# Kernel optimization log

Measured on AMD Instinct MI355X. Metric: run time of the kernel, lower is better.

The kernel has to match this reference:

```python
import jax, jax.numpy as jnp
import numpy as np

B, S, D, H, DH, F = 4, 2048, 1024, 16, 64, 4096
EPS = 1e-5


def setup_inputs() -> dict:
    key = jax.random.key(0)
    ks = jax.random.split(key, 8)
    std = 0.02
    return {
        "src": jax.random.normal(ks[0], (B, S, D), dtype=jnp.float32),
        # per-head Q/K/V projections, stacked: [H, D, DH]
        "Wq": jax.random.normal(ks[1], (H, D, DH), dtype=jnp.float32) * std,
        "bq": jnp.zeros((H, DH), dtype=jnp.float32),
        "Wk": jax.random.normal(ks[2], (H, D, DH), dtype=jnp.float32) * std,
        "bk": jnp.zeros((H, DH), dtype=jnp.float32),
        "Wv": jax.random.normal(ks[3], (H, D, DH), dtype=jnp.float32) * std,
        "bv": jnp.zeros((H, DH), dtype=jnp.float32),
        "Wo": jax.random.normal(ks[4], (H * DH, D), dtype=jnp.float32) * std,
        "bo": jnp.zeros((D,), dtype=jnp.float32),
        "ln1_w": jnp.ones((D,), dtype=jnp.float32),
        "ln1_b": jnp.zeros((D,), dtype=jnp.float32),
        "W1": jax.random.normal(ks[5], (D, F), dtype=jnp.float32) * std,
        "b1": jnp.zeros((F,), dtype=jnp.float32),
        "W2": jax.random.normal(ks[6], (F, D), dtype=jnp.float32) * std,
        "b2": jnp.zeros((D,), dtype=jnp.float32),
        "ln2_w": jnp.ones((D,), dtype=jnp.float32),
        "ln2_b": jnp.zeros((D,), dtype=jnp.float32),
    }


def _layernorm(x, w, b):
    m = jnp.mean(x, axis=-1, keepdims=True)
    v = jnp.mean(jnp.square(x - m), axis=-1, keepdims=True)
    return (x - m) * jax.lax.rsqrt(v + EPS) * w + b


def reference(src, Wq, bq, Wk, bk, Wv, bv, Wo, bo, ln1_w, ln1_b, W1, b1, W2, b2, ln2_w, ln2_b):
    # Per-head projections, batched over heads: [B,H,S,DH]
    q = jnp.einsum('bsd,hde->bhse', src, Wq) + bq[None, :, None, :]
    k = jnp.einsum('bsd,hde->bhse', src, Wk) + bk[None, :, None, :]
    v = jnp.einsum('bsd,hde->bhse', src, Wv) + bv[None, :, None, :]
    scale = jnp.asarray(DH, src.dtype) ** 0.5
    scores = jnp.einsum('bhqe,bhke->bhqk', q, k) / scale  # [B,H,S,S]
    attn = jax.nn.softmax(scores, axis=-1)
    ctx = jnp.einsum('bhqk,bhke->bhqe', attn, v)  # [B,H,S,DH]
    # concat heads along feature dim (matches torch.cat over head outputs)
    ctx = ctx.transpose(0, 2, 1, 3).reshape(src.shape[0], src.shape[1], H * DH)
    attn_out = ctx @ Wo + bo
    x = _layernorm(src + attn_out, ln1_w, ln1_b)
    ffn = jax.nn.relu(x @ W1 + b1) @ W2 + b2
    return _layernorm(x + ffn, ln2_w, ln2_b)
```

## Files before the change

### kernel.cpp

```cpp
#include <hip/hip_runtime.h>
#include <stdint.h>


typedef unsigned short u16;
typedef __attribute__((ext_vector_type(8))) short short8;
typedef __attribute__((ext_vector_type(4))) float f32x4;
typedef __attribute__((ext_vector_type(16))) float f32x16;

__device__ __forceinline__ u16 f2bf(float f) {
  union { float f; unsigned u; } v; v.f = f;
  unsigned r = (v.u + 0x7fffu + ((v.u >> 16) & 1u)) >> 16;
  return (u16)r;
}

__device__ __forceinline__ void gl_lds16(const u16* g, u16* l) {
  __builtin_amdgcn_global_load_lds(
      (const __attribute__((address_space(1))) unsigned int*)g,
      (__attribute__((address_space(3))) unsigned int*)l, 16, 0, 0);
}

__device__ __forceinline__ unsigned cvtpk(float lo, float hi) {
  unsigned r;
  asm("v_cvt_pk_bf16_f32 %0, %1, %2" : "=v"(r) : "v"(lo), "v"(hi));
  return r;
}
__device__ __forceinline__ void pl32_swap(unsigned& a, unsigned& b) {
  asm("v_permlane32_swap_b32 %0, %1" : "+v"(a), "+v"(b));
}


__global__ __launch_bounds__(256) void transpose_cast(const float* __restrict__ W,
                                                      u16* __restrict__ WT,
                                                      int K, int N) {
  __shared__ u16 T[64 * 72];
  const int tid = threadIdx.x;
  const long n0 = (long)blockIdx.x * 64, k0 = (long)blockIdx.y * 64;
#pragma unroll
  for (int i = 0; i < 4; i++) {
    int c = tid + i * 256;
    int kr = c >> 4, nc = (c & 15) * 4;
    float4 v = *(const float4*)(W + (k0 + kr) * N + n0 + nc);
    T[(nc + 0) * 72 + kr] = f2bf(v.x);
    T[(nc + 1) * 72 + kr] = f2bf(v.y);
    T[(nc + 2) * 72 + kr] = f2bf(v.z);
    T[(nc + 3) * 72 + kr] = f2bf(v.w);
  }
  __syncthreads();
#pragma unroll
  for (int i = 0; i < 2; i++) {
    int c = tid + i * 256;
    int nr = c >> 3, kc = (c & 7) * 8;
    *(uint4*)(WT + (n0 + nr) * K + k0 + kc) = *(const uint4*)(T + nr * 72 + kc);
  }
}

__global__ __launch_bounds__(256) void transpose_cast_qkv(const float* __restrict__ Wq,
                                                          const float* __restrict__ Wk,
                                                          const float* __restrict__ Wv,
                                                          u16* __restrict__ WT) {
  __shared__ u16 T[64 * 72];
  const int tid = threadIdx.x;
  const int n0 = blockIdx.x * 64, k0 = blockIdx.y * 64;
  const float* W = (n0 < 1024) ? Wq : (n0 < 2048 ? Wk : Wv);
  const int h = (n0 & 1023) >> 6;
#pragma unroll
  for (int i = 0; i < 4; i++) {
    int c = tid + i * 256;
    int kr = c >> 4, ec = (c & 15) * 4;
    float4 v = *(const float4*)(W + ((long)h * 1024 + k0 + kr) * 64 + ec);
    T[(ec + 0) * 72 + kr] = f2bf(v.x);
    T[(ec + 1) * 72 + kr] = f2bf(v.y);
    T[(ec + 2) * 72 + kr] = f2bf(v.z);
    T[(ec + 3) * 72 + kr] = f2bf(v.w);
  }
  __syncthreads();
#pragma unroll
  for (int i = 0; i < 2; i++) {
    int c = tid + i * 256;
    int nr = c >> 3, kc = (c & 7) * 8;
    *(uint4*)(WT + ((long)(n0 + nr)) * 1024 + k0 + kc) = *(const uint4*)(T + nr * 72 + kc);
  }
}

__global__ __launch_bounds__(256) void cast_bf16(const float* __restrict__ x, u16* __restrict__ y) {
  const long i = ((long)blockIdx.x * 256 + threadIdx.x) * 8;
  float4 a = *(const float4*)(x + i);
  float4 b = *(const float4*)(x + i + 4);
  uint4 o;
  o.x = (unsigned)f2bf(a.x) | ((unsigned)f2bf(a.y) << 16);
  o.y = (unsigned)f2bf(a.z) | ((unsigned)f2bf(a.w) << 16);
  o.z = (unsigned)f2bf(b.x) | ((unsigned)f2bf(b.y) << 16);
  o.w = (unsigned)f2bf(b.z) | ((unsigned)f2bf(b.w) << 16);
  *(uint4*)(y + i) = o;
}

__global__ __launch_bounds__(256) void build_bcat(const float* __restrict__ bq,
                                                  const float* __restrict__ bk,
                                                  const float* __restrict__ bv,
                                                  float* __restrict__ bcat) {
  int i = blockIdx.x * 256 + threadIdx.x;
  const float* s = (i < 1024) ? bq : (i < 2048 ? bk : bv);
  bcat[i] = s[i & 1023];
}

#define GEMM_PROLOGUE                                                              \
  __shared__ __align__(16) u16 As[2][4096];                                        \
  __shared__ __align__(16) u16 Bs[2][4096];                                        \
  const int tid = threadIdx.x;                                                     \
  const int wave = tid >> 6, lane = tid & 63, quad = lane >> 4, l15 = lane & 15;   \
  const int wm = (wave >> 1) * 64, wn = (wave & 1) * 64;                           \
  const int id = blockIdx.x, xcd = id & 7, ii = id >> 3;                           \
  const long m0 = (long)(xcd * 8 + (ii & 7)) * 128, n0 = (long)(ii >> 3) * 128;    \
  const int srow = tid >> 2, sc = (tid & 3) ^ ((srow >> 1) & 3);                   \
  const u16* Ag = A + (m0 + srow) * K + sc * 8;                                    \
  const u16* Bg = B + (n0 + srow) * K + sc * 8;                                    \
  const int cx = (l15 >> 1) & 3;                                                   \
  f32x4 acc[4][4] = {};                                                            \
  gl_lds16(Ag, &As[0][tid * 8]);                                                   \
  gl_lds16(Ag + (long)64 * K, &As[0][tid * 8 + 2048]);                             \
  gl_lds16(Bg, &Bs[0][tid * 8]);                                                   \
  gl_lds16(Bg + (long)64 * K, &Bs[0][tid * 8 + 2048]);                             \
  for (int k0 = 0; k0 < K; k0 += 32) {                                             \
    __syncthreads();         \
    const int cur = (k0 >> 5) & 1;                                                 \
    if (k0 + 32 < K) {                                                             \
      gl_lds16(Ag + k0 + 32, &As[cur ^ 1][tid * 8]);                               \
      gl_lds16(Ag + (long)64 * K + k0 + 32, &As[cur ^ 1][tid * 8 + 2048]);         \
      gl_lds16(Bg + k0 + 32, &Bs[cur ^ 1][tid * 8]);                               \
      gl_lds16(Bg + (long)64 * K + k0 + 32, &Bs[cur ^ 1][tid * 8 + 2048]);         \
    }                                                                              \
    short8 af[4], bfr[4];                                                          \
    _Pragma("unroll") for (int t = 0; t < 4; t++)                                  \
        af[t] = *(const short8*)(&As[cur][(wm + t * 16 + l15) * 32 + (quad ^ cx) * 8]); \
    _Pragma("unroll") for (int t = 0; t < 4; t++)                                  \
        bfr[t] = *(const short8*)(&Bs[cur][(wn + t * 16 + l15) * 32 + (quad ^ cx) * 8]); \
    _Pragma("unroll") for (int i = 0; i < 4; i++)                                  \
        _Pragma("unroll") for (int j = 0; j < 4; j++)                              \
            acc[i][j] = __builtin_amdgcn_mfma_f32_16x16x32_bf16(af[i], bfr[j],     \
                                                                acc[i][j], 0, 0, 0); \
  }

template <int MODE>
__global__ __launch_bounds__(256) void gemm_bt(const u16* __restrict__ A, const u16* __restrict__ B,
                                               const float* __restrict__ bias, void* __restrict__ Cout,
                                               int K, int N) {
  GEMM_PROLOGUE
#pragma unroll
  for (int i = 0; i < 4; i++) {
#pragma unroll
    for (int j = 0; j < 4; j++) {
      const long col = n0 + wn + j * 16 + l15;
      const float bb = bias[col];
      const long rowb = m0 + wm + i * 16 + quad * 4;
#pragma unroll
      for (int r = 0; r < 4; r++) {
        float v = acc[i][j][r] + bb;
        if (MODE == 2) v = fmaxf(v, 0.f);
        if (MODE == 0)
          ((float*)Cout)[(rowb + r) * N + col] = v;
        else
          ((u16*)Cout)[(rowb + r) * N + col] = f2bf(v);
      }
    }
  }
}

template <int MODE>
__global__ __launch_bounds__(512) void gemm_bt_sk(const u16* __restrict__ A, const u16* __restrict__ B,
                                                  const float* __restrict__ bias, void* __restrict__ Cout,
                                                  int K, int N) {
  __shared__ __align__(16) u16 As[2][2][4096];
  __shared__ __align__(16) u16 Bs[2][2][4096];
  const int tid = threadIdx.x;
  const int wave = tid >> 6, lane = tid & 63, quad = lane >> 4, l15 = lane & 15;
  const int kh = wave >> 2, w4 = wave & 3;
  const int wm = (w4 >> 1) * 64, wn = (w4 & 1) * 64;
  const int id = blockIdx.x, xcd = id & 7, ii = id >> 3;
  const long m0 = (long)(xcd * 8 + (ii & 7)) * 128, n0 = (long)(ii >> 3) * 128;
  const int t = tid & 255;
  const int srow = t >> 2, sc = (t & 3) ^ ((srow >> 1) & 3);
  const int Kh = K >> 1;
  const u16* Ag = A + (m0 + srow) * K + kh * Kh + sc * 8;
  const u16* Bg = B + (n0 + srow) * K + kh * Kh + sc * 8;
  const int cx = (l15 >> 1) & 3;
  f32x4 acc[4][4] = {};
  gl_lds16(Ag, &As[kh][0][t * 8]);
  gl_lds16(Ag + (long)64 * K, &As[kh][0][t * 8 + 2048]);
  gl_lds16(Bg, &Bs[kh][0][t * 8]);
  gl_lds16(Bg + (long)64 * K, &Bs[kh][0][t * 8 + 2048]);
  for (int k0 = 0; k0 < Kh; k0 += 32) {
    __syncthreads();
    const int cur = (k0 >> 5) & 1;
    if (k0 + 32 < Kh) {
      gl_lds16(Ag + k0 + 32, &As[kh][cur ^ 1][t * 8]);
      gl_lds16(Ag + (long)64 * K + k0 + 32, &As[kh][cur ^ 1][t * 8 + 2048]);
      gl_lds16(Bg + k0 + 32, &Bs[kh][cur ^ 1][t * 8]);
      gl_lds16(Bg + (long)64 * K + k0 + 32, &Bs[kh][cur ^ 1][t * 8 + 2048]);
    }
    short8 af[4], bfr[4];
#pragma unroll
    for (int tt = 0; tt < 4; tt++)
      af[tt] = *(const short8*)(&As[kh][cur][(wm + tt * 16 + l15) * 32 + (quad ^ cx) * 8]);
#pragma unroll
    for (int tt = 0; tt < 4; tt++)
      bfr[tt] = *(const short8*)(&Bs[kh][cur][(wn + tt * 16 + l15) * 32 + (quad ^ cx) * 8]);
#pragma unroll
    for (int i = 0; i < 4; i++)
#pragma unroll
      for (int j = 0; j < 4; j++)
        acc[i][j] = __builtin_amdgcn_mfma_f32_16x16x32_bf16(af[i], bfr[j], acc[i][j], 0, 0, 0);
  }
  __syncthreads();
  float* red = (w4 & 2) ? (float*)Bs : (float*)As;
  float* myred = red + (w4 & 1) * 4096 + lane * 4;
  if (kh == 1) {
#pragma unroll
    for (int i = 0; i < 4; i++)
#pragma unroll
      for (int j = 0; j < 4; j++)
        *(f32x4*)(myred + (i * 4 + j) * 256) = acc[i][j];
  }
  __syncthreads();
  if (kh == 0) {
#pragma unroll
    for (int i = 0; i < 4; i++) {
#pragma unroll
      for (int j = 0; j < 4; j++) {
        const f32x4 o = *(const f32x4*)(myred + (i * 4 + j) * 256);
        const long col = n0 + wn + j * 16 + l15;
        const float bb = bias[col];
        const long rowb = m0 + wm + i * 16 + quad * 4;
#pragma unroll
        for (int r = 0; r < 4; r++) {
          float v = acc[i][j][r] + o[r] + bb;
          if (MODE == 2) v = fmaxf(v, 0.f);
          if (MODE == 0)
            ((float*)Cout)[(rowb + r) * N + col] = v;
          else
            ((u16*)Cout)[(rowb + r) * N + col] = f2bf(v);
        }
      }
    }
  }
}

__global__ __launch_bounds__(256) void gemm_qkv(const u16* __restrict__ A, const u16* __restrict__ B,
                                                const float* __restrict__ bias,
                                                u16* __restrict__ QKb, u16* __restrict__ Vt, int K) {
  GEMM_PROLOGUE
#pragma unroll
  for (int i = 0; i < 4; i++) {
#pragma unroll
    for (int j = 0; j < 4; j++) {
      const int col0 = (int)n0 + wn + j * 16;
      const int col = col0 + l15;
      const float bb = bias[col];
      const long rowb = m0 + wm + i * 16 + quad * 4;
      if (col0 < 1024) {
#pragma unroll
        for (int r = 0; r < 4; r++)
          QKb[(rowb + r) * 2048 + col] = f2bf((acc[i][j][r] + bb) * 0.1803368801f);
      } else if (col0 < 2048) {
#pragma unroll
        for (int r = 0; r < 4; r++)
          QKb[(rowb + r) * 2048 + col] = f2bf(acc[i][j][r] + bb);
      } else {
        const int ec = col - 2048;
        const int bq = (int)(rowb >> 11), s = (int)(rowb & 2047);
        uint2 p;
        p.x = (unsigned)f2bf(acc[i][j][0] + bb) | ((unsigned)f2bf(acc[i][j][1] + bb) << 16);
        p.y = (unsigned)f2bf(acc[i][j][2] + bb) | ((unsigned)f2bf(acc[i][j][3] + bb) << 16);
        *(uint2*)(Vt + ((long)(bq * 16 + (ec >> 6)) * 64 + (ec & 63)) * 2048 + s) = p;
      }
    }
  }
}


__device__ __forceinline__ void stage_tile(const u16* __restrict__ g, u16* __restrict__ lds, int tid) {
#pragma unroll
  for (int i = 0; i < 2; i++) {
    const int s = i * 256 + tid;
    const int r = s >> 3, cs = s & 7;
    const int c = cs ^ (r & 7);
    gl_lds16(g + (long)r * 2048 + c * 8, lds + s * 8);
  }
}
__device__ __forceinline__ short8 frag(const u16* __restrict__ buf, int row, int chunk) {
  const int slot = row * 8 + (chunk ^ (row & 7));
  return *(const short8*)(buf + slot * 8);
}

__global__ __launch_bounds__(256, 2) void flash_attn(const u16* __restrict__ QKb,
                                                     const u16* __restrict__ Vt,
                                                     u16* __restrict__ ctx) {
  __shared__ __align__(16) u16 Kbuf[2][4096];
  __shared__ __align__(16) u16 Vbuf[2][4096];
  const int tid = threadIdx.x, wave = tid >> 6, lane = tid & 63;
  const int l31 = lane & 31, hi = lane >> 5;
  const int bh = blockIdx.x, b = bh >> 4, h = bh & 15;
  const int qt = blockIdx.y;
  const long qbase = (long)b * 2048 + qt * 256 + wave * 64;
  const u16* Qg = QKb + qbase * 2048 + h * 64;
  const u16* Kg = QKb + ((long)b * 2048) * 2048 + 1024 + h * 64;
  const u16* Vg = Vt + (long)bh * 64 * 2048;

  short8 qf[2][4];
#pragma unroll
  for (int j = 0; j < 2; j++)
#pragma unroll
    for (int ks = 0; ks < 4; ks++)
      qf[j][ks] = *(const short8*)(Qg + (long)(j * 32 + l31) * 2048 + ks * 16 + hi * 8);

  f32x16 O[2][2] = {};
  float rs[2] = {0.f, 0.f};

  stage_tile(Kg, Kbuf[0], tid);
  stage_tile(Vg, Vbuf[0], tid);

  for (int kt = 0; kt < 32; kt++) {
    __syncthreads();
    if (kt < 31) {
      stage_tile(Kg + (long)(kt + 1) * 64 * 2048, Kbuf[(kt + 1) & 1], tid);
      stage_tile(Vg + (kt + 1) * 64, Vbuf[(kt + 1) & 1], tid);
    }
    const u16* Kb = Kbuf[kt & 1];
    const u16* Vb = Vbuf[kt & 1];

#pragma unroll
    for (int m = 0; m < 2; m++) {
      short8 ak[4];
#pragma unroll
      for (int ks = 0; ks < 4; ks++) ak[ks] = frag(Kb, m * 32 + l31, ks * 2 + hi);
      f32x16 S[2] = {};
#pragma unroll
      for (int ks = 0; ks < 4; ks++)
#pragma unroll
        for (int j = 0; j < 2; j++)
          S[j] = __builtin_amdgcn_mfma_f32_32x32x16_bf16(ak[ks], qf[j][ks], S[j], 0, 0, 0);

      short8 pf[2][2];
#pragma unroll
      for (int j = 0; j < 2; j++) {
#pragma unroll
        for (int r = 0; r < 16; r++) S[j][r] = __builtin_amdgcn_exp2f(S[j][r]);
        rs[j] += ((S[j][0] + S[j][1]) + (S[j][2] + S[j][3])) +
                 ((S[j][4] + S[j][5]) + (S[j][6] + S[j][7])) +
                 ((S[j][8] + S[j][9]) + (S[j][10] + S[j][11])) +
                 ((S[j][12] + S[j][13]) + (S[j][14] + S[j][15]));
        unsigned w0 = cvtpk(S[j][0], S[j][1]), w1 = cvtpk(S[j][2], S[j][3]);
        unsigned w2 = cvtpk(S[j][4], S[j][5]), w3 = cvtpk(S[j][6], S[j][7]);
        unsigned w4 = cvtpk(S[j][8], S[j][9]), w5 = cvtpk(S[j][10], S[j][11]);
        unsigned w6 = cvtpk(S[j][12], S[j][13]), w7 = cvtpk(S[j][14], S[j][15]);
        pl32_swap(w2, w0); pl32_swap(w3, w1);
        pl32_swap(w6, w4); pl32_swap(w7, w5);
        union { unsigned u[4]; short8 s8; } f0, f1;
        f0.u[0] = w0; f0.u[1] = w1; f0.u[2] = w2; f0.u[3] = w3;
        f1.u[0] = w4; f1.u[1] = w5; f1.u[2] = w6; f1.u[3] = w7;
        pf[j][0] = f0.s8; pf[j][1] = f1.s8;
      }

#pragma unroll
      for (int et = 0; et < 2; et++) {
        short8 av[2];
#pragma unroll
        for (int ks2 = 0; ks2 < 2; ks2++)
          av[ks2] = frag(Vb, et * 32 + l31, m * 4 + ks2 * 2 + hi);
#pragma unroll
        for (int j = 0; j < 2; j++)
#pragma unroll
          for (int ks2 = 0; ks2 < 2; ks2++)
            O[et][j] = __builtin_amdgcn_mfma_f32_32x32x16_bf16(av[ks2], pf[j][ks2],
                                                               O[et][j], 0, 0, 0);
      }
    }
  }

#pragma unroll
  for (int j = 0; j < 2; j++) rs[j] += __shfl_xor(rs[j], 32);
#pragma unroll
  for (int j = 0; j < 2; j++) {
    const float inv = 1.f / rs[j];
    const long row = qbase + j * 32 + l31;
#pragma unroll
    for (int et = 0; et < 2; et++)
#pragma unroll
      for (int g = 0; g < 4; g++) {
        const int e0 = et * 32 + g * 8 + hi * 4;
        uint2 p;
        p.x = (unsigned)f2bf(O[et][j][g * 4 + 0] * inv) |
              ((unsigned)f2bf(O[et][j][g * 4 + 1] * inv) << 16);
        p.y = (unsigned)f2bf(O[et][j][g * 4 + 2] * inv) |
              ((unsigned)f2bf(O[et][j][g * 4 + 3] * inv) << 16);
        *(uint2*)(ctx + row * 1024 + h * 64 + e0) = p;
      }
  }
}

template <bool WB>
__global__ __launch_bounds__(256) void add_ln(const float* __restrict__ a, const float* __restrict__ c,
                                              const float* __restrict__ w, const float* __restrict__ bias,
                                              float* __restrict__ xout, u16* __restrict__ xbf) {
  const int row = blockIdx.x, tid = threadIdx.x;
  const long off = (long)row * 1024 + tid * 4;
  float4 va = *(const float4*)(a + off);
  float4 vc = *(const float4*)(c + off);
  float4 s = {va.x + vc.x, va.y + vc.y, va.z + vc.z, va.w + vc.w};
  float sum = s.x + s.y + s.z + s.w;
  float sq = s.x * s.x + s.y * s.y + s.z * s.z + s.w * s.w;
#pragma unroll
  for (int o = 32; o > 0; o >>= 1) {
    sum += __shfl_xor(sum, o);
    sq += __shfl_xor(sq, o);
  }
  __shared__ float red[8];
  const int wave = tid >> 6;
  if ((tid & 63) == 0) { red[wave] = sum; red[wave + 4] = sq; }
  __syncthreads();
  sum = red[0] + red[1] + red[2] + red[3];
  sq = red[4] + red[5] + red[6] + red[7];
  const float mean = sum * (1.f / 1024.f);
  const float var = sq * (1.f / 1024.f) - mean * mean;
  const float rstd = rsqrtf(var + 1e-5f);
  float4 vw = *(const float4*)(w + tid * 4);
  float4 vb = *(const float4*)(bias + tid * 4);
  float4 y;
  y.x = (s.x - mean) * rstd * vw.x + vb.x;
  y.y = (s.y - mean) * rstd * vw.y + vb.y;
  y.z = (s.z - mean) * rstd * vw.z + vb.z;
  y.w = (s.w - mean) * rstd * vw.w + vb.w;
  *(float4*)(xout + off) = y;
  if (WB) {
    uint2 o2;
    o2.x = (unsigned)f2bf(y.x) | ((unsigned)f2bf(y.y) << 16);
    o2.y = (unsigned)f2bf(y.z) | ((unsigned)f2bf(y.w) << 16);
    *(uint2*)(xbf + off) = o2;
  }
}

extern "C" void kernel_launch(void* const* d_in, const int* in_sizes, int n_in,
                              void* d_out, int out_size, void* d_ws, size_t ws_size,
                              hipStream_t stream) {
  (void)in_sizes; (void)n_in; (void)out_size; (void)ws_size;
  const float* src = (const float*)d_in[0];
  const float* Wq = (const float*)d_in[1];
  const float* bq = (const float*)d_in[2];
  const float* Wk = (const float*)d_in[3];
  const float* bk = (const float*)d_in[4];
  const float* Wv = (const float*)d_in[5];
  const float* bv = (const float*)d_in[6];
  const float* Wo = (const float*)d_in[7];
  const float* bo = (const float*)d_in[8];
  const float* ln1w = (const float*)d_in[9];
  const float* ln1b = (const float*)d_in[10];
  const float* W1 = (const float*)d_in[11];
  const float* b1 = (const float*)d_in[12];
  const float* W2 = (const float*)d_in[13];
  const float* b2 = (const float*)d_in[14];
  const float* ln2w = (const float*)d_in[15];
  const float* ln2b = (const float*)d_in[16];

  char* ws = (char*)d_ws;
  u16* WqkvT = (u16*)(ws + 0);
  u16* WoT = (u16*)(ws + (6ul << 20));
  u16* W1T = (u16*)(ws + (8ul << 20));
  u16* W2T = (u16*)(ws + (16ul << 20));
  float* bcat = (float*)(ws + (24ul << 20));
  u16* srcb = (u16*)(ws + (25ul << 20));
  u16* QKb = (u16*)(ws + (41ul << 20));
  u16* Vt = (u16*)(ws + (73ul << 20));
  u16* ctxb = (u16*)(ws + (89ul << 20));
  float* x = (float*)(ws + (105ul << 20));
  u16* xb = (u16*)(ws + (137ul << 20));
  u16* hb = (u16*)(ws + (41ul << 20));
  float* out = (float*)d_out;

  transpose_cast_qkv<<<dim3(48, 16), 256, 0, stream>>>(Wq, Wk, Wv, WqkvT);
  transpose_cast<<<dim3(16, 16), 256, 0, stream>>>(Wo, WoT, 1024, 1024);
  transpose_cast<<<dim3(64, 16), 256, 0, stream>>>(W1, W1T, 1024, 4096);
  transpose_cast<<<dim3(16, 64), 256, 0, stream>>>(W2, W2T, 4096, 1024);
  cast_bf16<<<4096, 256, 0, stream>>>(src, srcb);
  build_bcat<<<12, 256, 0, stream>>>(bq, bk, bv, bcat);

  gemm_qkv<<<24 * 64, 256, 0, stream>>>(srcb, WqkvT, bcat, QKb, Vt, 1024);
  flash_attn<<<dim3(64, 8), 256, 0, stream>>>(QKb, Vt, ctxb);
  gemm_bt_sk<0><<<8 * 64, 512, 0, stream>>>(ctxb, WoT, bo, out, 1024, 1024);
  add_ln<true><<<8192, 256, 0, stream>>>(src, out, ln1w, ln1b, x, xb);
  gemm_bt<2><<<32 * 64, 256, 0, stream>>>(xb, W1T, b1, hb, 1024, 4096);
  gemm_bt_sk<0><<<8 * 64, 512, 0, stream>>>(hb, W2T, b2, out, 4096, 1024);
  add_ln<false><<<8192, 256, 0, stream>>>(x, out, ln2w, ln2b, out, nullptr);
}
```

Baseline: 511.6 us.

## Triple-buffer GEMM LDS staging with explicit vmcnt waits and hoist bias loads

Turns the 256-thread GEMM k-loop from double to triple buffering, so tiles are prefetched two iterations ahead. It waits on the outstanding global-to-LDS loads with an explicit s_waitcnt vmcnt plus a raw s_barrier, where it previously relied on __syncthreads. Bias values are now loaded before the k-loop instead of in the epilogue. The goal is to hide global load latency better, at the cost of more LDS per block (48KB), which may lower occupancy. It also depends on the vmcnt count matching exactly four loads per stage.

```diff
diff --git a/kernel.cpp b/kernel.cpp
--- a/kernel.cpp
+++ b/kernel.cpp
@@ -103,9 +103,9 @@
   bcat[i] = s[i & 1023];
 }
 
-#define GEMM_PROLOGUE                                                              \
-  __shared__ __align__(16) u16 As[2][4096];                                        \
-  __shared__ __align__(16) u16 Bs[2][4096];                                        \
+#define GEMM_SETUP                                                                 \
+  __shared__ __align__(16) u16 As[3][4096];                                        \
+  __shared__ __align__(16) u16 Bs[3][4096];                                        \
   const int tid = threadIdx.x;                                                     \
   const int wave = tid >> 6, lane = tid & 63, quad = lane >> 4, l15 = lane & 15;   \
   const int wm = (wave >> 1) * 64, wn = (wave & 1) * 64;                           \
@@ -114,47 +114,59 @@
   const int srow = tid >> 2, sc = (tid & 3) ^ ((srow >> 1) & 3);                   \
   const u16* Ag = A + (m0 + srow) * K + sc * 8;                                    \
   const u16* Bg = B + (n0 + srow) * K + sc * 8;                                    \
-  const int cx = (l15 >> 1) & 3;                                                   \
-  f32x4 acc[4][4] = {};                                                            \
-  gl_lds16(Ag, &As[0][tid * 8]);                                                   \
-  gl_lds16(Ag + (long)64 * K, &As[0][tid * 8 + 2048]);                             \
-  gl_lds16(Bg, &Bs[0][tid * 8]);                                                   \
-  gl_lds16(Bg + (long)64 * K, &Bs[0][tid * 8 + 2048]);                             \
+  const int cq = quad ^ ((l15 >> 1) & 3);                                          \
+  f32x4 acc[4][4] = {};
+
+#define GEMM_STAGE(b, kof)                                                         \
+  {                                                                                \
+    gl_lds16(Ag + (kof), &As[b][tid * 8]);                                         \
+    gl_lds16(Ag + (long)64 * K + (kof), &As[b][tid * 8 + 2048]);                   \
+    gl_lds16(Bg + (kof), &Bs[b][tid * 8]);                                         \
+    gl_lds16(Bg + (long)64 * K + (kof), &Bs[b][tid * 8 + 2048]);                   \
+  }
+
+#define GEMM_KLOOP                                                                 \
+  GEMM_STAGE(0, 0)                                                                 \
+  GEMM_STAGE(1, 32)                                                                \
+  int cur = 0;                                                                     \
   for (int k0 = 0; k0 < K; k0 += 32) {                                             \
-    __syncthreads();         \
-    const int cur = (k0 >> 5) & 1;                                                 \
-    if (k0 + 32 < K) {                                                             \
-      gl_lds16(Ag + k0 + 32, &As[cur ^ 1][tid * 8]);                               \
-      gl_lds16(Ag + (long)64 * K + k0 + 32, &As[cur ^ 1][tid * 8 + 2048]);         \
-      gl_lds16(Bg + k0 + 32, &Bs[cur ^ 1][tid * 8]);                               \
-      gl_lds16(Bg + (long)64 * K + k0 + 32, &Bs[cur ^ 1][tid * 8 + 2048]);         \
+    if (k0 + 32 < K) asm volatile("s_waitcnt vmcnt(4)" ::: "memory");              \
+    else asm volatile("s_waitcnt vmcnt(0)" ::: "memory");                          \
+    __builtin_amdgcn_s_barrier();                                                  \
+    if (k0 + 64 < K) {                                                             \
+      const int nb = cur == 0 ? 2 : cur - 1;                        \
+      GEMM_STAGE(nb, k0 + 64)                                                      \
     }                                                                              \
     short8 af[4], bfr[4];                                                          \
     _Pragma("unroll") for (int t = 0; t < 4; t++)                                  \
-        af[t] = *(const short8*)(&As[cur][(wm + t * 16 + l15) * 32 + (quad ^ cx) * 8]); \
+        af[t] = *(const short8*)(&As[cur][(wm + t * 16 + l15) * 32 + cq * 8]);     \
     _Pragma("unroll") for (int t = 0; t < 4; t++)                                  \
-        bfr[t] = *(const short8*)(&Bs[cur][(wn + t * 16 + l15) * 32 + (quad ^ cx) * 8]); \
+        bfr[t] = *(const short8*)(&Bs[cur][(wn + t * 16 + l15) * 32 + cq * 8]);    \
     _Pragma("unroll") for (int i = 0; i < 4; i++)                                  \
         _Pragma("unroll") for (int j = 0; j < 4; j++)                              \
             acc[i][j] = __builtin_amdgcn_mfma_f32_16x16x32_bf16(af[i], bfr[j],     \
                                                                 acc[i][j], 0, 0, 0); \
+    cur = cur == 2 ? 0 : cur + 1;                                                  \
   }
 
 template <int MODE>
 __global__ __launch_bounds__(256) void gemm_bt(const u16* __restrict__ A, const u16* __restrict__ B,
                                                const float* __restrict__ bias, void* __restrict__ Cout,
                                                int K, int N) {
-  GEMM_PROLOGUE
+  GEMM_SETUP
+  float bb[4];
+#pragma unroll
+  for (int j = 0; j < 4; j++) bb[j] = bias[n0 + wn + j * 16 + l15];
+  GEMM_KLOOP
 #pragma unroll
   for (int i = 0; i < 4; i++) {
 #pragma unroll
     for (int j = 0; j < 4; j++) {
       const long col = n0 + wn + j * 16 + l15;
-      const float bb = bias[col];
       const long rowb = m0 + wm + i * 16 + quad * 4;
 #pragma unroll
       for (int r = 0; r < 4; r++) {
-        float v = acc[i][j][r] + bb;
+        float v = acc[i][j][r] + bb[j];
         if (MODE == 2) v = fmaxf(v, 0.f);
         if (MODE == 0)
           ((float*)Cout)[(rowb + r) * N + col] = v;
@@ -247,29 +259,32 @@
 __global__ __launch_bounds__(256) void gemm_qkv(const u16* __restrict__ A, const u16* __restrict__ B,
                                                 const float* __restrict__ bias,
                                                 u16* __restrict__ QKb, u16* __restrict__ Vt, int K) {
-  GEMM_PROLOGUE
+  GEMM_SETUP
+  float bb[4];
+#pragma unroll
+  for (int j = 0; j < 4; j++) bb[j] = bias[n0 + wn + j * 16 + l15];
+  GEMM_KLOOP
 #pragma unroll
   for (int i = 0; i < 4; i++) {
 #pragma unroll
     for (int j = 0; j < 4; j++) {
       const int col0 = (int)n0 + wn + j * 16;
       const int col = col0 + l15;
-      const float bb = bias[col];
       const long rowb = m0 + wm + i * 16 + quad * 4;
       if (col0 < 1024) {
 #pragma unroll
         for (int r = 0; r < 4; r++)
-          QKb[(rowb + r) * 2048 + col] = f2bf((acc[i][j][r] + bb) * 0.1803368801f);
+          QKb[(rowb + r) * 2048 + col] = f2bf((acc[i][j][r] + bb[j]) * 0.1803368801f);
       } else if (col0 < 2048) {
 #pragma unroll
         for (int r = 0; r < 4; r++)
-          QKb[(rowb + r) * 2048 + col] = f2bf(acc[i][j][r] + bb);
+          QKb[(rowb + r) * 2048 + col] = f2bf(acc[i][j][r] + bb[j]);
       } else {
         const int ec = col - 2048;
         const int bq = (int)(rowb >> 11), s = (int)(rowb & 2047);
         uint2 p;
-        p.x = (unsigned)f2bf(acc[i][j][0] + bb) | ((unsigned)f2bf(acc[i][j][1] + bb) << 16);
-        p.y = (unsigned)f2bf(acc[i][j][2] + bb) | ((unsigned)f2bf(acc[i][j][3] + bb) << 16);
+        p.x = (unsigned)f2bf(acc[i][j][0] + bb[j]) | ((unsigned)f2bf(acc[i][j][1] + bb[j]) << 16);
+        p.y = (unsigned)f2bf(acc[i][j][2] + bb[j]) | ((unsigned)f2bf(acc[i][j][3] + bb[j]) << 16);
         *(uint2*)(Vt + ((long)(bq * 16 + (ec >> 6)) * 64 + (ec & 63)) * 2048 + s) = p;
       }
     }
```

Result: no change. 513.1 us (+0.3%).
